# Performance work log

Hardware: AMD Instinct MI355X
Metric: run time of the kernel (lower is better)

Reference implementation:

```python
import jax, jax.numpy as jnp
import numpy as np

N_FREQS = 6  # PositionEmbedding default used by LISA


def setup_inputs() -> dict:
    key = jax.random.key(0)
    ks = jax.random.split(key, 8)
    B, L, N, D, H = 8, 32768, 2048, 64, 256
    in_dim = 1 * (2 * N_FREQS + 1) + 3 * D  # 13 + 192 = 205

    def w(k, i, o):
        return jax.random.normal(k, (i, o), jnp.float32) * (1.0 / np.sqrt(i))

    return {
        "coord": jax.random.uniform(ks[0], (B, L, 1), jnp.float32),
        "latent": jax.random.normal(ks[1], (B, N, D), jnp.float32),
        "W0": w(ks[2], in_dim, H), "b0": jnp.zeros((H,), jnp.float32),
        "W1": w(ks[3], H, H), "b1": jnp.zeros((H,), jnp.float32),
        "W2": w(ks[4], H, H), "b2": jnp.zeros((H,), jnp.float32),
        "W3": w(ks[5], H, H), "b3": jnp.zeros((H,), jnp.float32),
        "W4": w(ks[6], H, 1), "b4": jnp.zeros((1,), jnp.float32),
    }


def reference(coord, latent, W0, b0, W1, b1, W2, b2, W3, b3, W4, b4):
    B, N, D = latent.shape
    # feat_unfold: concat shifted-prev / self / shifted-next along channels
    feat = jnp.swapaxes(latent, 1, 2)                                   # [B, D, N]
    feat_prev = jnp.concatenate([feat[:, :, :1], feat[:, :, :-1]], axis=2)
    feat_next = jnp.concatenate([feat[:, :, 1:], feat[:, :, -1:]], axis=2)
    feat = jnp.concatenate([feat_prev, feat, feat_next], axis=1)        # [B, 3D, N]

    # grid_sample(bilinear, padding_mode='border', align_corners=False) on a
    # 1-row image: y coordinate 0 hits row 0 exactly, so only x interpolates.
    # torch mapping: ix = ((gx + 1) * W - 1) / 2 with gx = coord*2 - 1
    ix = coord[..., 0] * N - 0.5                                        # [B, L]
    x0 = jnp.floor(ix)
    t = ix - x0                                                         # lerp weight
    i0 = jnp.clip(x0.astype(jnp.int32), 0, N - 1)                       # border clamp
    i1 = jnp.clip(x0.astype(jnp.int32) + 1, 0, N - 1)
    f0 = jnp.take_along_axis(feat, i0[:, None, :], axis=2)              # [B, 3D, L]
    f1 = jnp.take_along_axis(feat, i1[:, None, :], axis=2)
    sampled = (1.0 - t)[:, None, :] * f0 + t[:, None, :] * f1
    sampled = jnp.swapaxes(sampled, 1, 2)                               # [B, L, 3D]

    # positional encoding: [x, sin(f x), cos(f x) for f in 1,2,4,8,16,32]
    freqs = 2.0 ** jnp.arange(N_FREQS, dtype=jnp.float32)
    ang = coord * freqs                                                 # [B, L, 6]
    pe = jnp.stack([jnp.sin(ang), jnp.cos(ang)], axis=-1)
    pe = pe.reshape(ang.shape[0], ang.shape[1], 2 * N_FREQS)            # [B, L, 12]

    inp = jnp.concatenate([coord, pe, sampled], axis=-1)                # [B, L, 205]

    h = jax.nn.relu(inp @ W0 + b0)
    h = jax.nn.relu(h @ W1 + b1)
    h = jax.nn.relu(h @ W2 + b2)
    h = jax.nn.relu(h @ W3 + b3)
    return h @ W4 + b4                                                  # [B, L, 1]
```

## Files before the change

### kernel.cpp

```cpp
#include <hip/hip_runtime.h>
#include <hip/hip_bf16.h>

typedef unsigned short ushort_t;
typedef unsigned int uint_t;
typedef __attribute__((ext_vector_type(8))) short short8;
typedef __attribute__((ext_vector_type(4))) float float4v;
typedef __attribute__((ext_vector_type(4))) uint_t uint4v;

#define NLAT 2048
#define DLAT 64

#define PW_BASE 128
#define PW0_OFF 0
#define PW1_OFF 57344
#define PW2_OFF 122880
#define PW3_OFF 188416

__device__ __forceinline__ float b2f(ushort_t u) {
  union { uint_t i; float f; } v; v.i = ((uint_t)u) << 16; return v.f;
}
__device__ __forceinline__ ushort_t f2b(float f) {
  uint_t x = __float_as_uint(f);
  uint_t r = (x + 0x7fffu + ((x >> 16) & 1u)) >> 16;
  return (ushort_t)r;
}
__device__ __forceinline__ uint_t pack2(float lo, float hi) {
  float2 t; t.x = lo; t.y = hi;
  union { __hip_bfloat162 h; uint_t u; } cv;
  cv.h = __float22bfloat162_rn(t);
  return cv.u;
}
__device__ __forceinline__ int imin(int a, int b) { return a < b ? a : b; }
__device__ __forceinline__ int imax(int a, int b) { return a > b ? a : b; }

__device__ __forceinline__ float ldv(const float* p, long i)    { return p[i]; }
__device__ __forceinline__ float ldv(const ushort_t* p, long i) { return b2f(p[i]); }
__device__ __forceinline__ void stv(float* p, long i, float v)    { p[i] = v; }
__device__ __forceinline__ void stv(ushort_t* p, long i, float v) { p[i] = f2b(v); }

__device__ __forceinline__ float4 load4f(const float* p) { return *(const float4*)p; }
__device__ __forceinline__ float4 load4f(const ushort_t* p) {
  uint2 u = *(const uint2*)p;
  float4 r;
  r.x = b2f((ushort_t)(u.x & 0xffffu)); r.y = b2f((ushort_t)(u.x >> 16));
  r.z = b2f((ushort_t)(u.y & 0xffffu)); r.w = b2f((ushort_t)(u.y >> 16));
  return r;
}

__global__ void detect_mode(const ushort_t* __restrict__ lat, int* __restrict__ flag) {
  if (threadIdx.x == 0) *flag = 0;
  __syncthreads();
  int big = 0;
  for (int i = threadIdx.x; i < 1024; i += 64) {
    float v = b2f(lat[i]);
    if (!(fabsf(v) < 1e5f)) big = 1;
  }
  if (__any(big) && threadIdx.x == 0) *flag = 1;
}

template <typename TI>
__global__ void pack_w_t(const TI* __restrict__ W0, const TI* __restrict__ W1,
                         const TI* __restrict__ W2, const TI* __restrict__ W3,
                         ushort_t* __restrict__ pw, const int* __restrict__ flag, int want)
{
  if (*flag != want) return;
  int g = blockIdx.x * blockDim.x + threadIdx.x;
  if (g >= 31 * 1024) return;
  int lane = g & 63, q = lane >> 4;
  int mt   = (g >> 6) & 15;
  int ktg  = g >> 10;
  const TI* W; ushort_t* dst; int kt, KT; bool isw0 = false;
  if (ktg < 7)       { W = W0; dst = pw + PW0_OFF; kt = ktg;      KT = 7; isw0 = true; }
  else if (ktg < 15) { W = W1; dst = pw + PW1_OFF; kt = ktg - 7;  KT = 8; }
  else if (ktg < 23) { W = W2; dst = pw + PW2_OFF; kt = ktg - 15; KT = 8; }
  else               { W = W3; dst = pw + PW3_OFF; kt = ktg - 23; KT = 8; }
  int col = mt * 16 + (lane & 15);
  uint_t words[4];
#pragma unroll
  for (int h = 0; h < 4; ++h) {
    ushort_t vv[2];
#pragma unroll
    for (int e = 0; e < 2; ++e) {
      int j = 2 * h + e;
      int f = 32 * kt + 16 * (j >> 2) + 4 * q + (j & 3);
      int row = f;
      if (isw0) row = (f < 192) ? (13 + f) : (f == 192 ? 0 : (f <= 204 ? f - 192 : -1));
      vv[e] = (row >= 0) ? f2b(ldv(W, (long)row * 256 + col)) : (ushort_t)0;
    }
    words[h] = (uint_t)vv[0] | ((uint_t)vv[1] << 16);
  }
  uint4 o; o.x = words[0]; o.y = words[1]; o.z = words[2]; o.w = words[3];
  *(uint4*)(dst + ((size_t)(mt * KT + kt) * 64 + lane) * 8) = o;
}

template <int KT>
__device__ __forceinline__ void prefetch_A0(const ushort_t* __restrict__ pwl,
                                            short8 (&A0)[4], int lane, int wv)
{
  const ushort_t* abase = pwl + (((size_t)(4 * wv) * KT) * 64 + lane) * 8;
#pragma unroll
  for (int m = 0; m < 4; ++m)
    A0[m] = *(const short8*)(abase + (size_t)(m * KT) * 512);
}

template <int KT>
__device__ __forceinline__ void run_layer_new(const ushort_t* __restrict__ pwl,
                                              float4v (&acc)[4][4],
                                              const ushort_t* __restrict__ act,
                                              int lane, int wv, short8 (&A0)[4])
{
#pragma unroll
  for (int m = 0; m < 4; ++m)
#pragma unroll
    for (int i = 0; i < 4; ++i)
      acc[m][i] = (float4v){0.f, 0.f, 0.f, 0.f};

  const ushort_t* abase = pwl + (((size_t)(4 * wv) * KT) * 64 + lane) * 8;
  short8 A1[4], B0[4], B1[4];

  int boff[4];
#pragma unroll
  for (int i = 0; i < 4; ++i) boff[i] = (((wv + i) & 3) << 12) + (lane << 3);

#pragma unroll
  for (int i = 0; i < 4; ++i)
    B0[i] = *(const short8*)&act[boff[i]];

#pragma unroll
  for (int kt = 0; kt < KT; ++kt) {
    short8 (&Ac)[4] = (kt & 1) ? A1 : A0;
    short8 (&An)[4] = (kt & 1) ? A0 : A1;
    short8 (&Bc)[4] = (kt & 1) ? B1 : B0;
    short8 (&Bn)[4] = (kt & 1) ? B0 : B1;
    if (kt + 1 < KT) {
#pragma unroll
      for (int m = 0; m < 4; ++m)
        An[m] = *(const short8*)(abase + (size_t)(m * KT + kt + 1) * 512);
#pragma unroll
      for (int i = 0; i < 4; ++i)
        Bn[i] = *(const short8*)&act[boff[i] + (kt + 1) * 512];
    }
    __builtin_amdgcn_s_setprio(1);
#pragma unroll
    for (int i = 0; i < 4; ++i) {
      acc[0][i] = __builtin_amdgcn_mfma_f32_16x16x32_bf16(Ac[0], Bc[i], acc[0][i], 0, 0, 0);
      acc[1][i] = __builtin_amdgcn_mfma_f32_16x16x32_bf16(Ac[1], Bc[i], acc[1][i], 0, 0, 0);
      acc[2][i] = __builtin_amdgcn_mfma_f32_16x16x32_bf16(Ac[2], Bc[i], acc[2][i], 0, 0, 0);
      acc[3][i] = __builtin_amdgcn_mfma_f32_16x16x32_bf16(Ac[3], Bc[i], acc[3][i], 0, 0, 0);
    }
    __builtin_amdgcn_s_setprio(0);
  }
}

__device__ __forceinline__ void convert_store(float4v (&acc)[4][4],
                                              ushort_t* __restrict__ actN,
                                              const float* __restrict__ bwl,
                                              int lane, int wv, int q)
{
#pragma unroll
  for (int p2 = 0; p2 < 2; ++p2) {
    const float4 bE = *(const float4*)&bwl[wv * 64 + p2 * 32 + 4 * q];
    const float4 bO = *(const float4*)&bwl[wv * 64 + p2 * 32 + 16 + 4 * q];
    const int kt = 2 * wv + p2;
#pragma unroll
    for (int i = 0; i < 4; ++i) {
      const int p = (wv + i) & 3;
      const float4v& aE = acc[2 * p2][i];
      const float4v& aO = acc[2 * p2 + 1][i];
      uint4 o;
      o.x = pack2(fmaxf(aE[0] + bE.x, 0.f), fmaxf(aE[1] + bE.y, 0.f));
      o.y = pack2(fmaxf(aE[2] + bE.z, 0.f), fmaxf(aE[3] + bE.w, 0.f));
      o.z = pack2(fmaxf(aO[0] + bO.x, 0.f), fmaxf(aO[1] + bO.y, 0.f));
      o.w = pack2(fmaxf(aO[2] + bO.z, 0.f), fmaxf(aO[3] + bO.w, 0.f));
      *(uint4*)&actN[(size_t)(p << 12) + kt * 512 + (lane << 3)] = o;
    }
  }
  asm volatile("s_waitcnt lgkmcnt(0)" ::: "memory");
  __builtin_amdgcn_s_barrier();
}

template <typename TI>
__global__ __launch_bounds__(256, 2) void lisa_fused_t(
    const TI* __restrict__ coord, const TI* __restrict__ latent,
    const TI* __restrict__ bias0, const TI* __restrict__ bias1,
    const TI* __restrict__ bias2, const TI* __restrict__ bias3,
    const TI* __restrict__ W4,    const TI* __restrict__ b4,
    const ushort_t* __restrict__ pw, TI* __restrict__ out,
    const int* __restrict__ flag, int want)
{
  if (*flag != want) return;
  __shared__ __align__(16) ushort_t act[2][4 * 8 * 64 * 8];
  __shared__ __align__(16) float bw[4 * 256 + 256 + 1];

  const int tid  = threadIdx.x;
  const int lane = tid & 63, q = lane >> 4, m15 = lane & 15;
  const int wv   = tid >> 6;
  const long pbase = (long)blockIdx.x * 64 + wv * 16 + m15;

  short8 A0[4];
  prefetch_A0<7>(pw + PW0_OFF, A0, lane, wv);

  for (int i = tid; i < 1281; i += 256) {
    float v;
    if (i < 256)       v = ldv(bias0, i);
    else if (i < 512)  v = ldv(bias1, i - 256);
    else if (i < 768)  v = ldv(bias2, i - 512);
    else if (i < 1024) v = ldv(bias3, i - 768);
    else if (i < 1280) v = ldv(W4, i - 1024);
    else               v = ldv(b4, 0);
    bw[i] = v;
  }

  {
    const long p = pbase;
    float c   = ldv(coord, p);
    float ixv = c * 2048.0f - 0.5f;
    float x0f = floorf(ixv);
    float t   = ixv - x0f;
    int   x0  = (int)x0f;
    int   i0  = imin(imax(x0, 0), NLAT - 1);
    int   i1  = imin(imax(x0 + 1, 0), NLAT - 1);
    float w0 = 1.0f - t, w1 = t;
    int rows0[3] = { imax(i0 - 1, 0), i0, imin(i0 + 1, NLAT - 1) };
    int rows1[3] = { imax(i1 - 1, 0), i1, imin(i1 + 1, NLAT - 1) };
    const TI* lat = latent + (size_t)(p >> 15) * (NLAT * DLAT);
    uint4v hu[7];
#pragma unroll
    for (int tb = 0; tb < 12; ++tb) {
      int region = tb >> 2;
      int d0 = 16 * (tb & 3) + 4 * q;
      float4 a = load4f(lat + (long)rows0[region] * DLAT + d0);
      float4 b = load4f(lat + (long)rows1[region] * DLAT + d0);
      hu[tb >> 1][(tb & 1) * 2 + 0] = pack2(w0 * a.x + w1 * b.x, w0 * a.y + w1 * b.y);
      hu[tb >> 1][(tb & 1) * 2 + 1] = pack2(w0 * a.z + w1 * b.z, w0 * a.w + w1 * b.w);
    }
    float pv[4];
#pragma unroll
    for (int s = 0; s < 4; ++s) {
      int f = 192 + 4 * q + s;
      float v = 0.0f;
      if (f == 192) v = c;
      else if (f <= 204) {
        int i = f - 193;
        float fr = (float)(1 << (i >> 1));
        float ang = c * fr;
        v = (i & 1) ? __cosf(ang) : __sinf(ang);
      }
      pv[s] = v;
    }
    hu[6][0] = pack2(pv[0], pv[1]);
    hu[6][1] = pack2(pv[2], pv[3]);
    hu[6][2] = 0; hu[6][3] = 0;

#pragma unroll
    for (int kt = 0; kt < 7; ++kt)
      *(uint4v*)&act[0][((size_t)(wv * 8 + kt) * 64 + lane) * 8] = hu[kt];
  }
  __syncthreads();

  float4v acc[4][4];

  run_layer_new<7>(pw + PW0_OFF, acc, act[0], lane, wv, A0);
  prefetch_A0<8>(pw + PW1_OFF, A0, lane, wv);
  convert_store(acc, act[1], bw + 0 * 256, lane, wv, q);
  run_layer_new<8>(pw + PW1_OFF, acc, act[1], lane, wv, A0);
  prefetch_A0<8>(pw + PW2_OFF, A0, lane, wv);
  convert_store(acc, act[0], bw + 1 * 256, lane, wv, q);
  run_layer_new<8>(pw + PW2_OFF, acc, act[0], lane, wv, A0);
  prefetch_A0<8>(pw + PW3_OFF, A0, lane, wv);
  convert_store(acc, act[1], bw + 2 * 256, lane, wv, q);
  run_layer_new<8>(pw + PW3_OFF, acc, act[1], lane, wv, A0);

  float psum[4] = {0.f, 0.f, 0.f, 0.f};
#pragma unroll
  for (int m = 0; m < 4; ++m) {
    const float4 b3v = *(const float4*)&bw[3 * 256 + wv * 64 + m * 16 + 4 * q];
    const float4 w4v = *(const float4*)&bw[1024 + wv * 64 + m * 16 + 4 * q];
#pragma unroll
    for (int i = 0; i < 4; ++i) {
      float v;
      v = fmaxf(acc[m][i][0] + b3v.x, 0.f); psum[i] += v * w4v.x;
      v = fmaxf(acc[m][i][1] + b3v.y, 0.f); psum[i] += v * w4v.y;
      v = fmaxf(acc[m][i][2] + b3v.z, 0.f); psum[i] += v * w4v.z;
      v = fmaxf(acc[m][i][3] + b3v.w, 0.f); psum[i] += v * w4v.w;
    }
  }
#pragma unroll
  for (int i = 0; i < 4; ++i) {
    psum[i] += __shfl_xor(psum[i], 16, 64);
    psum[i] += __shfl_xor(psum[i], 32, 64);
  }

  float* part = (float*)act[0];
  if (lane < 16) {
#pragma unroll
    for (int i = 0; i < 4; ++i) {
      const int p = (wv + i) & 3;
      part[wv * 64 + p * 16 + lane] = psum[i];
    }
  }
  __syncthreads();
  if (tid < 64) {
    float s = part[tid] + part[64 + tid] + part[128 + tid] + part[192 + tid]
            + bw[1280];
    stv(out, (long)blockIdx.x * 64 + tid, s);
  }
}

extern "C" void kernel_launch(void* const* d_in, const int* in_sizes, int n_in,
                              void* d_out, int out_size, void* d_ws, size_t ws_size,
                              hipStream_t stream) {
  int* flag = (int*)d_ws;
  ushort_t* pw = (ushort_t*)d_ws + PW_BASE;

  detect_mode<<<1, 64, 0, stream>>>((const ushort_t*)d_in[1], flag);

  pack_w_t<float><<<62, 512, 0, stream>>>(
      (const float*)d_in[2], (const float*)d_in[4], (const float*)d_in[6],
      (const float*)d_in[8], pw, flag, 1);
  lisa_fused_t<float><<<4096, 256, 0, stream>>>(
      (const float*)d_in[0], (const float*)d_in[1],
      (const float*)d_in[3], (const float*)d_in[5], (const float*)d_in[7],
      (const float*)d_in[9], (const float*)d_in[10], (const float*)d_in[11],
      pw, (float*)d_out, flag, 1);

  pack_w_t<ushort_t><<<62, 512, 0, stream>>>(
      (const ushort_t*)d_in[2], (const ushort_t*)d_in[4], (const ushort_t*)d_in[6],
      (const ushort_t*)d_in[8], pw, flag, 0);
  lisa_fused_t<ushort_t><<<4096, 256, 0, stream>>>(
      (const ushort_t*)d_in[0], (const ushort_t*)d_in[1],
      (const ushort_t*)d_in[3], (const ushort_t*)d_in[5], (const ushort_t*)d_in[7],
      (const ushort_t*)d_in[9], (const ushort_t*)d_in[10], (const ushort_t*)d_in[11],
      pw, (ushort_t*)d_out, flag, 0);
}
```

Baseline: 229.5 us.

## Deepen weight-fragment prefetch with asm loads and cross-layer ring buffer

Weight A-fragments are now loaded two k-steps ahead into a 4-slot register ring, using inline-asm global_load_dwordx4 with explicit s_waitcnt vmcnt counts. The last steps of each layer issue the first fragments of the next layer, so the loads run under the MFMAs across layer boundaries. The goal is to hide global/L2 latency on weight fetches that the previous one-step double buffer left exposed. It adds register pressure and depends on manual vmcnt accounting that the compiler cannot check. A barrier is also added before LDS scratch reuse.

```diff
diff --git a/kernel.cpp b/kernel.cpp
--- a/kernel.cpp
+++ b/kernel.cpp
@@ -45,6 +45,17 @@
   r.x = b2f((ushort_t)(u.x & 0xffffu)); r.y = b2f((ushort_t)(u.x >> 16));
   r.z = b2f((ushort_t)(u.y & 0xffffu)); r.w = b2f((ushort_t)(u.y >> 16));
   return r;
+}
+
+__device__ __forceinline__ void aload(short8& dst, const ushort_t* a) {
+  asm volatile("global_load_dwordx4 %0, %1, off" : "=v"(dst) : "v"(a));
+}
+template <int N>
+__device__ __forceinline__ void vmwait() {
+  if constexpr (N == 0)      asm volatile("s_waitcnt vmcnt(0)" ::: "memory");
+  else if constexpr (N == 4) asm volatile("s_waitcnt vmcnt(4)" ::: "memory");
+  else                       asm volatile("s_waitcnt vmcnt(8)" ::: "memory");
+  __builtin_amdgcn_sched_barrier(0);
 }
 
 __global__ void detect_mode(const ushort_t* __restrict__ lat, int* __restrict__ flag) {
@@ -94,20 +105,21 @@
 }
 
 template <int KT>
-__device__ __forceinline__ void prefetch_A0(const ushort_t* __restrict__ pwl,
-                                            short8 (&A0)[4], int lane, int wv)
+__device__ __forceinline__ void issueA(const ushort_t* __restrict__ pwl,
+                                       short8 (&dst)[4], int kt, int lane, int wv)
 {
   const ushort_t* abase = pwl + (((size_t)(4 * wv) * KT) * 64 + lane) * 8;
 #pragma unroll
   for (int m = 0; m < 4; ++m)
-    A0[m] = *(const short8*)(abase + (size_t)(m * KT) * 512);
-}
-
-template <int KT>
-__device__ __forceinline__ void run_layer_new(const ushort_t* __restrict__ pwl,
+    aload(dst[m], abase + (size_t)(m * KT + kt) * 512);
+}
+
+template <int KT, int BASE, int NEXTKT>
+__device__ __forceinline__ void run_layer_asm(const ushort_t* __restrict__ pwl,
+                                              const ushort_t* __restrict__ pwl_next,
                                               float4v (&acc)[4][4],
                                               const ushort_t* __restrict__ act,
-                                              int lane, int wv, short8 (&A0)[4])
+                                              int lane, int wv, short8 (&Ar)[4][4])
 {
 #pragma unroll
   for (int m = 0; m < 4; ++m)
@@ -115,31 +127,33 @@
     for (int i = 0; i < 4; ++i)
       acc[m][i] = (float4v){0.f, 0.f, 0.f, 0.f};
 
-  const ushort_t* abase = pwl + (((size_t)(4 * wv) * KT) * 64 + lane) * 8;
-  short8 A1[4], B0[4], B1[4];
-
+  short8 B0[4], B1[4];
   int boff[4];
 #pragma unroll
   for (int i = 0; i < 4; ++i) boff[i] = (((wv + i) & 3) << 12) + (lane << 3);
-
 #pragma unroll
   for (int i = 0; i < 4; ++i)
     B0[i] = *(const short8*)&act[boff[i]];
 
 #pragma unroll
   for (int kt = 0; kt < KT; ++kt) {
-    short8 (&Ac)[4] = (kt & 1) ? A1 : A0;
-    short8 (&An)[4] = (kt & 1) ? A0 : A1;
+    if (kt + 2 < KT) {
+      issueA<KT>(pwl, Ar[(BASE + kt + 2) & 3], kt + 2, lane, wv);
+    } else {
+      if constexpr (NEXTKT > 0)
+        issueA<NEXTKT>(pwl_next, Ar[(BASE + kt + 2) & 3], kt + 2 - KT, lane, wv);
+    }
     short8 (&Bc)[4] = (kt & 1) ? B1 : B0;
     short8 (&Bn)[4] = (kt & 1) ? B0 : B1;
     if (kt + 1 < KT) {
 #pragma unroll
-      for (int m = 0; m < 4; ++m)
-        An[m] = *(const short8*)(abase + (size_t)(m * KT + kt + 1) * 512);
-#pragma unroll
       for (int i = 0; i < 4; ++i)
         Bn[i] = *(const short8*)&act[boff[i] + (kt + 1) * 512];
     }
+    if (kt + 2 < KT || NEXTKT > 0) vmwait<8>();
+    else if (kt + 1 < KT)          vmwait<4>();
+    else                           vmwait<0>();
+    short8 (&Ac)[4] = Ar[(BASE + kt) & 3];
     __builtin_amdgcn_s_setprio(1);
 #pragma unroll
     for (int i = 0; i < 4; ++i) {
@@ -196,9 +210,6 @@
   const int lane = tid & 63, q = lane >> 4, m15 = lane & 15;
   const int wv   = tid >> 6;
   const long pbase = (long)blockIdx.x * 64 + wv * 16 + m15;
-
-  short8 A0[4];
-  prefetch_A0<7>(pw + PW0_OFF, A0, lane, wv);
 
   for (int i = tid; i < 1281; i += 256) {
     float v;
@@ -258,18 +269,19 @@
   }
   __syncthreads();
 
+  short8 Ar[4][4];
+  issueA<7>(pw + PW0_OFF, Ar[0], 0, lane, wv);
+  issueA<7>(pw + PW0_OFF, Ar[1], 1, lane, wv);
+
   float4v acc[4][4];
 
-  run_layer_new<7>(pw + PW0_OFF, acc, act[0], lane, wv, A0);
-  prefetch_A0<8>(pw + PW1_OFF, A0, lane, wv);
+  run_layer_asm<7, 0, 8>(pw + PW0_OFF, pw + PW1_OFF, acc, act[0], lane, wv, Ar);
   convert_store(acc, act[1], bw + 0 * 256, lane, wv, q);
-  run_layer_new<8>(pw + PW1_OFF, acc, act[1], lane, wv, A0);
-  prefetch_A0<8>(pw + PW2_OFF, A0, lane, wv);
+  run_layer_asm<8, 3, 8>(pw + PW1_OFF, pw + PW2_OFF, acc, act[1], lane, wv, Ar);
   convert_store(acc, act[0], bw + 1 * 256, lane, wv, q);
-  run_layer_new<8>(pw + PW2_OFF, acc, act[0], lane, wv, A0);
-  prefetch_A0<8>(pw + PW3_OFF, A0, lane, wv);
+  run_layer_asm<8, 3, 8>(pw + PW2_OFF, pw + PW3_OFF, acc, act[0], lane, wv, Ar);
   convert_store(acc, act[1], bw + 2 * 256, lane, wv, q);
-  run_layer_new<8>(pw + PW3_OFF, acc, act[1], lane, wv, A0);
+  run_layer_asm<8, 3, 0>(pw + PW3_OFF, nullptr,      acc, act[1], lane, wv, Ar);
 
   float psum[4] = {0.f, 0.f, 0.f, 0.f};
 #pragma unroll
@@ -291,6 +303,8 @@
     psum[i] += __shfl_xor(psum[i], 32, 64);
   }
 
+  asm volatile("" ::: "memory");
+  __builtin_amdgcn_s_barrier();
   float* part = (float*)act[0];
   if (lane < 16) {
 #pragma unroll
```

Result: no change. 226.8 us (-1.2%).
